# Performance work log

Measured on AMD Instinct MI355X. Metric: run time of the kernel, lower is better.

## Reference

```python
import jax, jax.numpy as jnp
import numpy as np

B, C, N = 8, 256, 4096
K = C // 4  # projection dim for F and G (feat_dim // 4)


def setup_inputs() -> dict:
    key = jax.random.key(0)
    k1, k2, k3, k4, k5, k6 = jax.random.split(key, 6)
    inp = {
        "input": jax.random.normal(k1, (B, C, N), dtype=jnp.float32),
        "nms_feat": jax.random.normal(k2, (B, C, N), dtype=jnp.float32),
        "WF": jax.random.normal(k3, (K, C), dtype=jnp.float32) * (1.0 / np.sqrt(C)),
        "WG": jax.random.normal(k4, (K, C), dtype=jnp.float32) * (1.0 / np.sqrt(C)),
        "WH": jax.random.normal(k5, (C, C), dtype=jnp.float32) * (1.0 / np.sqrt(C)),
        "gamma": jax.random.normal(k6, (1,), dtype=jnp.float32),
    }
    return inp


def reference(input, nms_feat, WF, WG, WH, gamma):
    feat = nms_feat  # [B, C, N]; module uses nms_feat when provided
    b, c, n = feat.shape
    # 1x1 conv projections == channel matmuls; outputs laid out as [B, N, d]
    f = jnp.einsum('kc,bcn->bnk', WF, feat)   # [B, N, K]
    g = jnp.einsum('kc,bcn->bnk', WG, feat)   # [B, N, K]
    h = jnp.einsum('dc,bcn->bnd', WH, feat)   # [B, N, C]
    # attention scores (no scaling in original module)
    s = jnp.einsum('bnk,bmk->bnm', g, f)      # [B, N, N]
    beta = jax.nn.softmax(s, axis=-1)
    o = jnp.einsum('bnm,bmd->bnd', beta, h)   # [B, N, C]
    # NOTE: the original does a raw reshape [B,N,C] -> [B,C,N] (not a transpose);
    # we reproduce that exactly.
    o = o.reshape(b, c, n)
    return gamma * o + input
```

## Files before the change

### kernel.cpp

```cpp
#include <hip/hip_runtime.h>
#include <hip/hip_bf16.h>

#define BB 8
#define CC 256
#define NN 4096
#define KP 64
#define LOG2E 1.44269504088896f

typedef _Float16 f16x8 __attribute__((ext_vector_type(8)));
typedef _Float16 f16x4 __attribute__((ext_vector_type(4)));
typedef float    f32x4 __attribute__((ext_vector_type(4)));

#define MFMA16(a, b, c) __builtin_amdgcn_mfma_f32_16x16x32_f16((a), (b), (c), 0, 0, 0)

__device__ __forceinline__ float fast_exp2(float x) {
#if __has_builtin(__builtin_amdgcn_exp2f)
    return __builtin_amdgcn_exp2f(x);
#else
    return __expf(x * 0.69314718055994531f);
#endif
}

template<int CTRL>
__device__ __forceinline__ float dpp_ror_f(float x) {
    return __int_as_float(__builtin_amdgcn_update_dpp(
        0, __float_as_int(x), CTRL, 0xF, 0xF, true));
}
__device__ __forceinline__ float max16(float x) {
    x = fmaxf(x, dpp_ror_f<0x128>(x));
    x = fmaxf(x, dpp_ror_f<0x124>(x));
    x = fmaxf(x, dpp_ror_f<0x122>(x));
    x = fmaxf(x, dpp_ror_f<0x121>(x));
    return x;
}
__device__ __forceinline__ float sum16(float x) {
    x += dpp_ror_f<0x128>(x);
    x += dpp_ror_f<0x124>(x);
    x += dpp_ror_f<0x122>(x);
    x += dpp_ror_f<0x121>(x);
    return x;
}

__global__ __launch_bounds__(256) void wconv_kernel(
    const float* __restrict__ WF, const float* __restrict__ WG,
    const float* __restrict__ WH, _Float16* __restrict__ W16)
{
    int gid = blockIdx.x * 256 + threadIdx.x;
    int i4  = gid * 4;
    const float* src;
    if (i4 < 64 * CC)        src = WF + i4;
    else if (i4 < 128 * CC)  src = WG + (i4 - 64 * CC);
    else                     src = WH + (i4 - 128 * CC);
    float4 v = *(const float4*)src;
    f16x4 o = { (_Float16)v.x, (_Float16)v.y, (_Float16)v.z, (_Float16)v.w };
    *(f16x4*)(W16 + i4) = o;
}

__global__ __launch_bounds__(256, 3) void proj16_kernel(
    const float* __restrict__ feat, const _Float16* __restrict__ W16,
    _Float16* __restrict__ fb, _Float16* __restrict__ gb,
    _Float16* __restrict__ hT)
{
    __shared__ __align__(16) _Float16 ft[64][264];
    const int b = blockIdx.y, n0 = blockIdx.x * 64, t = threadIdx.x;

    #pragma unroll
    for (int i = 0; i < 16; i++) {
        int v = t + i * 256, c = v >> 4, nq = v & 15;
        float4 x = *(const float4*)(feat + ((size_t)b * CC + c) * NN + n0 + nq * 4);
        ft[nq * 4 + 0][c] = (_Float16)x.x;
        ft[nq * 4 + 1][c] = (_Float16)x.y;
        ft[nq * 4 + 2][c] = (_Float16)x.z;
        ft[nq * 4 + 3][c] = (_Float16)x.w;
    }
    __syncthreads();

    const int w = t >> 6, lane = t & 63, quad = lane >> 4, ln = lane & 15;
    const int rowbase = w * 96;

    f32x4 acc[6][4] = {};
    #pragma unroll
    for (int ks = 0; ks < 8; ks++) {
        const int c0 = ks * 32;
        f16x8 bfr[4];
        #pragma unroll
        for (int tf = 0; tf < 4; tf++)
            bfr[tf] = *(const f16x8*)&ft[tf * 16 + ln][c0 + quad * 8];
        #pragma unroll
        for (int af = 0; af < 6; af++) {
            f16x8 a = *(const f16x8*)(W16 + (size_t)(rowbase + af * 16 + ln) * CC + c0 + quad * 8);
            #pragma unroll
            for (int tf = 0; tf < 4; tf++)
                acc[af][tf] = MFMA16(a, bfr[tf], acc[af][tf]);
        }
    }

    #pragma unroll
    for (int af = 0; af < 6; af++) {
        const int orow0 = rowbase + af * 16 + quad * 4;
        if (orow0 < 64) {
            #pragma unroll
            for (int tf = 0; tf < 4; tf++) {
                const int tok = n0 + tf * 16 + ln;
                f16x4 pk = { (_Float16)acc[af][tf][0], (_Float16)acc[af][tf][1],
                             (_Float16)acc[af][tf][2], (_Float16)acc[af][tf][3] };
                *(f16x4*)(fb + ((size_t)b * NN + tok) * KP + orow0) = pk;
            }
        } else if (orow0 < 128) {
            #pragma unroll
            for (int tf = 0; tf < 4; tf++) {
                const int tok = n0 + tf * 16 + ln;
                f16x4 pk = { (_Float16)(acc[af][tf][0] * LOG2E),
                             (_Float16)(acc[af][tf][1] * LOG2E),
                             (_Float16)(acc[af][tf][2] * LOG2E),
                             (_Float16)(acc[af][tf][3] * LOG2E) };
                *(f16x4*)(gb + ((size_t)b * NN + tok) * KP + (orow0 - 64)) = pk;
            }
        } else {
            #pragma unroll
            for (int r = 0; r < 4; r++) {
                const int d = orow0 - 128 + r;
                f16x4 pk = { (_Float16)acc[af][0][r], (_Float16)acc[af][1][r],
                             (_Float16)acc[af][2][r], (_Float16)acc[af][3][r] };
                *(f16x4*)(hT + ((size_t)b * CC + d) * NN + n0 + ln * 4) = pk;
            }
        }
    }
}

__global__ __launch_bounds__(256, 2) void attn16_kernel(
    const _Float16* __restrict__ fb, const _Float16* __restrict__ gb,
    const _Float16* __restrict__ hT, const float* __restrict__ inp,
    const float* __restrict__ gamma, float* __restrict__ out)
{
    __shared__ __align__(16) _Float16 g_s[64][72];
    __shared__ __align__(16) _Float16 f_s[64][72];
    __shared__ __align__(16) _Float16 p_s[64][72];
    __shared__ float alpha_s[64];
    __shared__ float l_s[64];
    __shared__ float chg_s[4];

    const int b = blockIdx.x, q0 = blockIdx.y * 64, t = threadIdx.x;
    const int w = t >> 6, lane = t & 63, quad = lane >> 4, ln = lane & 15;
    const int row = t >> 2, kq = t & 3;
    const int dbase = w * 64;

    {
        const _Float16* src = gb + ((size_t)b * NN + q0 + row) * KP + kq * 16;
        *(f16x8*)&g_s[row][kq * 16]     = *(const f16x8*)(src);
        *(f16x8*)&g_s[row][kq * 16 + 8] = *(const f16x8*)(src + 8);
    }
    f16x8 fr0, fr1;
    {
        const _Float16* src = fb + ((size_t)b * NN + row) * KP + kq * 16;
        fr0 = *(const f16x8*)(src);
        fr1 = *(const f16x8*)(src + 8);
    }
    __syncthreads();

    f16x8 ag[2];
    ag[0] = *(const f16x8*)&g_s[w * 16 + ln][quad * 8];
    ag[1] = *(const f16x8*)&g_s[w * 16 + ln][32 + quad * 8];

    float m_run[4] = {-1e30f, -1e30f, -1e30f, -1e30f};
    float l_run[4] = {0.f, 0.f, 0.f, 0.f};
    f32x4 acc[4][4] = {};
    f16x8 hv[2][4];

    #pragma unroll 1
    for (int mt = 0; mt < NN / 64; mt++) {
        const int m0 = mt * 64;

        *(f16x8*)&f_s[row][kq * 16]     = fr0;
        *(f16x8*)&f_s[row][kq * 16 + 8] = fr1;
        __syncthreads();

        {
            const int m0n = ((mt + 1) & 63) * 64;
            const _Float16* srcf = fb + ((size_t)b * NN + m0n + row) * KP + kq * 16;
            fr0 = *(const f16x8*)(srcf);
            fr1 = *(const f16x8*)(srcf + 8);
            #pragma unroll
            for (int ks = 0; ks < 2; ks++)
                #pragma unroll
                for (int df = 0; df < 4; df++)
                    hv[ks][df] = *(const f16x8*)(hT +
                        ((size_t)b * CC + dbase + df * 16 + ln) * NN + m0 + ks * 32 + quad * 8);
        }

        f32x4 S[4] = {};
        #pragma unroll
        for (int ks = 0; ks < 2; ks++) {
            #pragma unroll
            for (int mf = 0; mf < 4; mf++) {
                f16x8 bf = *(const f16x8*)&f_s[mf * 16 + ln][ks * 32 + quad * 8];
                S[mf] = MFMA16(ag[ks], bf, S[mf]);
            }
        }

        float pmax[4];
        bool upd = false;
        #pragma unroll
        for (int r = 0; r < 4; r++) {
            pmax[r] = fmaxf(fmaxf(S[0][r], S[1][r]), fmaxf(S[2][r], S[3][r]));
            upd |= (pmax[r] > m_run[r] + 10.0f);
        }
        const bool wave_upd = (__ballot(upd) != 0ull);
        if (wave_upd) {
            #pragma unroll
            for (int r = 0; r < 4; r++) {
                float mx   = max16(pmax[r]);
                float mnew = fmaxf(m_run[r], mx);
                float al   = fast_exp2(m_run[r] - mnew);
                l_run[r] *= al;
                m_run[r]  = mnew;
                if (ln == 0) alpha_s[w * 16 + quad * 4 + r] = al;
            }
        }
        if (lane == 0) chg_s[w] = wave_upd ? 1.0f : 0.0f;
        #pragma unroll
        for (int r = 0; r < 4; r++) {
            float p0 = fast_exp2(S[0][r] - m_run[r]);
            float p1 = fast_exp2(S[1][r] - m_run[r]);
            float p2 = fast_exp2(S[2][r] - m_run[r]);
            float p3 = fast_exp2(S[3][r] - m_run[r]);
            l_run[r] += (p0 + p1) + (p2 + p3);
            f16x4 pk = { (_Float16)p0, (_Float16)p1, (_Float16)p2, (_Float16)p3 };
            *(f16x4*)&p_s[w * 16 + quad * 4 + r][ln * 4] = pk;
        }
        __syncthreads();

        {
            float c0 = chg_s[0], c1 = chg_s[1], c2 = chg_s[2], c3 = chg_s[3];
            float chg[4] = {c0, c1, c2, c3};
            #pragma unroll
            for (int qf = 0; qf < 4; qf++) {
                if (chg[qf] != 0.0f) {
                    #pragma unroll
                    for (int r = 0; r < 4; r++) {
                        float al = alpha_s[qf * 16 + quad * 4 + r];
                        #pragma unroll
                        for (int df = 0; df < 4; df++)
                            acc[qf][df][r] *= al;
                    }
                }
            }
        }

        #pragma unroll
        for (int ks = 0; ks < 2; ks++) {
            #pragma unroll
            for (int qf = 0; qf < 4; qf++) {
                f16x8 ap = *(const f16x8*)&p_s[qf * 16 + ln][ks * 32 + quad * 8];
                #pragma unroll
                for (int df = 0; df < 4; df++)
                    acc[qf][df] = MFMA16(ap, hv[ks][df], acc[qf][df]);
            }
        }
    }

    #pragma unroll
    for (int r = 0; r < 4; r++) {
        float lt = sum16(l_run[r]);
        if (ln == 0) l_s[w * 16 + quad * 4 + r] = lt;
    }
    __syncthreads();

    const float gam = gamma[0];
    #pragma unroll
    for (int qf = 0; qf < 4; qf++) {
        #pragma unroll
        for (int r = 0; r < 4; r++) {
            const int q = qf * 16 + quad * 4 + r;
            const float linv = 1.0f / l_s[q];
            #pragma unroll
            for (int df = 0; df < 4; df++) {
                const int d = dbase + df * 16 + ln;
                size_t idx = ((size_t)b * NN + q0 + q) * CC + d;
                out[idx] = fmaf(gam, acc[qf][df][r] * linv, inp[idx]);
            }
        }
    }
}

extern "C" void kernel_launch(void* const* d_in, const int* in_sizes, int n_in,
                              void* d_out, int out_size, void* d_ws, size_t ws_size,
                              hipStream_t stream) {
    const float* input = (const float*)d_in[0];
    const float* nms   = (const float*)d_in[1];
    const float* WF    = (const float*)d_in[2];
    const float* WG    = (const float*)d_in[3];
    const float* WH    = (const float*)d_in[4];
    const float* gamma = (const float*)d_in[5];
    float* out = (float*)d_out;

    char* ws = (char*)d_ws;
    _Float16* W16  = (_Float16*)ws;
    _Float16* fb16 = (_Float16*)(ws + 196608);
    _Float16* gb16 = (_Float16*)(ws + 196608 + 4194304);
    _Float16* hT16 = (_Float16*)(ws + 196608 + 2 * 4194304);

    wconv_kernel<<<96, 256, 0, stream>>>(WF, WG, WH, W16);
    proj16_kernel<<<dim3(NN / 64, BB), 256, 0, stream>>>(nms, W16, fb16, gb16, hT16);
    attn16_kernel<<<dim3(BB, NN / 64), 256, 0, stream>>>(fb16, gb16, hT16, input, gamma, out);
}
```

Before: 255.9 us.

## Split attention key range across two blocks and merge with log-sum-exp combine

```diff
diff --git a/kernel.cpp b/kernel.cpp
--- a/kernel.cpp
+++ b/kernel.cpp
@@ -128,11 +128,14 @@
     }
 }
 
-__global__ __launch_bounds__(256, 2) void attn16_kernel(
+template<int NSPLIT>
+__global__ __launch_bounds__(256, 4) void attn16_kernel(
     const _Float16* __restrict__ fb, const _Float16* __restrict__ gb,
     const _Float16* __restrict__ hT, const float* __restrict__ inp,
-    const float* __restrict__ gamma, float* __restrict__ out)
+    const float* __restrict__ gamma, float* __restrict__ out,
+    _Float16* __restrict__ oP, float* __restrict__ lseP)
 {
+    constexpr int ITERS = (NN / 64) / NSPLIT;
     __shared__ __align__(16) _Float16 g_s[64][72];
     __shared__ __align__(16) _Float16 f_s[64][72];
     __shared__ __align__(16) _Float16 p_s[64][72];
@@ -141,6 +144,8 @@
     __shared__ float chg_s[4];
 
     const int b = blockIdx.x, q0 = blockIdx.y * 64, t = threadIdx.x;
+    const int z = (NSPLIT > 1) ? blockIdx.z : 0;
+    const int mtbase = z * ITERS;
     const int w = t >> 6, lane = t & 63, quad = lane >> 4, ln = lane & 15;
     const int row = t >> 2, kq = t & 3;
     const int dbase = w * 64;
@@ -152,7 +157,7 @@
     }
     f16x8 fr0, fr1;
     {
-        const _Float16* src = fb + ((size_t)b * NN + row) * KP + kq * 16;
+        const _Float16* src = fb + ((size_t)b * NN + mtbase * 64 + row) * KP + kq * 16;
         fr0 = *(const f16x8*)(src);
         fr1 = *(const f16x8*)(src + 8);
     }
@@ -168,15 +173,15 @@
     f16x8 hv[2][4];
 
     #pragma unroll 1
-    for (int mt = 0; mt < NN / 64; mt++) {
-        const int m0 = mt * 64;
+    for (int mtl = 0; mtl < ITERS; mtl++) {
+        const int m0 = (mtbase + mtl) * 64;
 
         *(f16x8*)&f_s[row][kq * 16]     = fr0;
         *(f16x8*)&f_s[row][kq * 16 + 8] = fr1;
         __syncthreads();
 
         {
-            const int m0n = ((mt + 1) & 63) * 64;
+            const int m0n = (mtbase + ((mtl + 1) & (ITERS - 1))) * 64;
             const _Float16* srcf = fb + ((size_t)b * NN + m0n + row) * KP + kq * 16;
             fr0 = *(const f16x8*)(srcf);
             fr1 = *(const f16x8*)(srcf + 8);
@@ -231,8 +236,7 @@
         __syncthreads();
 
         {
-            float c0 = chg_s[0], c1 = chg_s[1], c2 = chg_s[2], c3 = chg_s[3];
-            float chg[4] = {c0, c1, c2, c3};
+            float chg[4] = { chg_s[0], chg_s[1], chg_s[2], chg_s[3] };
             #pragma unroll
             for (int qf = 0; qf < 4; qf++) {
                 if (chg[qf] != 0.0f) {
@@ -262,25 +266,83 @@
     #pragma unroll
     for (int r = 0; r < 4; r++) {
         float lt = sum16(l_run[r]);
-        if (ln == 0) l_s[w * 16 + quad * 4 + r] = lt;
+        if (ln == 0) {
+            l_s[w * 16 + quad * 4 + r] = lt;
+            if (NSPLIT > 1)
+                lseP[(size_t)z * BB * NN + (size_t)b * NN + q0 + w * 16 + quad * 4 + r]
+                    = m_run[r] + __log2f(lt);
+        }
     }
     __syncthreads();
 
+    if constexpr (NSPLIT == 1) {
+        const float gam = gamma[0];
+        #pragma unroll
+        for (int qf = 0; qf < 4; qf++) {
+            #pragma unroll
+            for (int r = 0; r < 4; r++) {
+                const int q = qf * 16 + quad * 4 + r;
+                const float linv = 1.0f / l_s[q];
+                #pragma unroll
+                for (int df = 0; df < 4; df++) {
+                    const int d = dbase + df * 16 + ln;
+                    size_t idx = ((size_t)b * NN + q0 + q) * CC + d;
+                    out[idx] = fmaf(gam, acc[qf][df][r] * linv, inp[idx]);
+                }
+            }
+        }
+    } else {
+        _Float16* oPz = oP + (size_t)z * BB * NN * CC;
+        #pragma unroll
+        for (int qf = 0; qf < 4; qf++) {
+            #pragma unroll
+            for (int r = 0; r < 4; r++) {
+                const int q = qf * 16 + quad * 4 + r;
+                const float linv = 1.0f / l_s[q];
+                #pragma unroll
+                for (int df = 0; df < 4; df++) {
+                    const int d = dbase + df * 16 + ln;
+                    oPz[((size_t)b * NN + q0 + q) * CC + d] = (_Float16)(acc[qf][df][r] * linv);
+                }
+            }
+        }
+    }
+}
+
+__global__ __launch_bounds__(256) void combine_kernel(
+    const _Float16* __restrict__ oP, const float* __restrict__ lseP,
+    const float* __restrict__ inp, const float* __restrict__ gamma,
+    float* __restrict__ out)
+{
+    const int gid = blockIdx.x * 256 + threadIdx.x;
+    const int rowi = gid >> 5;
+    const int d0 = (gid & 31) * 8;
+    const size_t base = (size_t)rowi * CC + d0;
+
+    float l0 = lseP[rowi];
+    float l1 = lseP[(size_t)BB * NN + rowi];
+    float M  = fmaxf(l0, l1);
+    float w0 = fast_exp2(l0 - M), w1 = fast_exp2(l1 - M);
+    float inv = 1.0f / (w0 + w1);
+    w0 *= inv; w1 *= inv;
+
+    f16x8 a0 = *(const f16x8*)(oP + base);
+    f16x8 a1 = *(const f16x8*)(oP + (size_t)BB * NN * CC + base);
     const float gam = gamma[0];
-    #pragma unroll
-    for (int qf = 0; qf < 4; qf++) {
-        #pragma unroll
-        for (int r = 0; r < 4; r++) {
-            const int q = qf * 16 + quad * 4 + r;
-            const float linv = 1.0f / l_s[q];
-            #pragma unroll
-            for (int df = 0; df < 4; df++) {
-                const int d = dbase + df * 16 + ln;
-                size_t idx = ((size_t)b * NN + q0 + q) * CC + d;
-                out[idx] = fmaf(gam, acc[qf][df][r] * linv, inp[idx]);
-            }
-        }
-    }
+
+    float4 i0 = *(const float4*)(inp + base);
+    float4 i1 = *(const float4*)(inp + base + 4);
+    float4 o0, o1;
+    o0.x = fmaf(gam, w0 * (float)a0[0] + w1 * (float)a1[0], i0.x);
+    o0.y = fmaf(gam, w0 * (float)a0[1] + w1 * (float)a1[1], i0.y);
+    o0.z = fmaf(gam, w0 * (float)a0[2] + w1 * (float)a1[2], i0.z);
+    o0.w = fmaf(gam, w0 * (float)a0[3] + w1 * (float)a1[3], i0.w);
+    o1.x = fmaf(gam, w0 * (float)a0[4] + w1 * (float)a1[4], i1.x);
+    o1.y = fmaf(gam, w0 * (float)a0[5] + w1 * (float)a1[5], i1.y);
+    o1.z = fmaf(gam, w0 * (float)a0[6] + w1 * (float)a1[6], i1.z);
+    o1.w = fmaf(gam, w0 * (float)a0[7] + w1 * (float)a1[7], i1.w);
+    *(float4*)(out + base)     = o0;
+    *(float4*)(out + base + 4) = o1;
 }
 
 extern "C" void kernel_launch(void* const* d_in, const int* in_sizes, int n_in,
@@ -299,8 +361,21 @@
     _Float16* fb16 = (_Float16*)(ws + 196608);
     _Float16* gb16 = (_Float16*)(ws + 196608 + 4194304);
     _Float16* hT16 = (_Float16*)(ws + 196608 + 2 * 4194304);
+    const size_t base_end = 196608 + 2 * 4194304 + (size_t)2 * BB * NN * CC;
+    _Float16* oP   = (_Float16*)(ws + base_end);
+    float*    lseP = (float*)(ws + base_end + (size_t)2 * 2 * BB * NN * CC);
+    const size_t need = base_end + (size_t)2 * 2 * BB * NN * CC + (size_t)2 * 4 * BB * NN;
 
     wconv_kernel<<<96, 256, 0, stream>>>(WF, WG, WH, W16);
     proj16_kernel<<<dim3(NN / 64, BB), 256, 0, stream>>>(nms, W16, fb16, gb16, hT16);
-    attn16_kernel<<<dim3(BB, NN / 64), 256, 0, stream>>>(fb16, gb16, hT16, input, gamma, out);
-}
+
+    if (ws_size >= need) {
+        attn16_kernel<2><<<dim3(BB, NN / 64, 2), 256, 0, stream>>>(
+            fb16, gb16, hT16, input, gamma, out, oP, lseP);
+        combine_kernel<<<(BB * NN * CC / 8) / 256, 256, 0, stream>>>(
+            oP, lseP, input, gamma, out);
+    } else {
+        attn16_kernel<1><<<dim3(BB, NN / 64), 256, 0, stream>>>(
+            fb16, gb16, hT16, input, gamma, out, oP, lseP);
+    }
+}
```

Measured after the change: 552.6 us. 2.16x slower.

## Halve query tile to 32 rows, raise occupancy, split h loads

Applied to the files above, without the earlier changes.

```diff
diff --git a/kernel.cpp b/kernel.cpp
--- a/kernel.cpp
+++ b/kernel.cpp
@@ -128,27 +128,27 @@
     }
 }
 
-__global__ __launch_bounds__(256, 2) void attn16_kernel(
+__global__ __launch_bounds__(256, 4) void attn16_kernel(
     const _Float16* __restrict__ fb, const _Float16* __restrict__ gb,
     const _Float16* __restrict__ hT, const float* __restrict__ inp,
     const float* __restrict__ gamma, float* __restrict__ out)
 {
-    __shared__ __align__(16) _Float16 g_s[64][72];
+    __shared__ __align__(16) _Float16 g_s[32][72];
     __shared__ __align__(16) _Float16 f_s[64][72];
-    __shared__ __align__(16) _Float16 p_s[64][72];
-    __shared__ float alpha_s[64];
-    __shared__ float l_s[64];
-    __shared__ float chg_s[4];
-
-    const int b = blockIdx.x, q0 = blockIdx.y * 64, t = threadIdx.x;
+    __shared__ __align__(16) _Float16 p_s[32][72];
+    __shared__ float alpha_s[32];
+    __shared__ float l_s[32];
+    __shared__ float chg_s[2];
+
+    const int b = blockIdx.x, q0 = blockIdx.y * 32, t = threadIdx.x;
     const int w = t >> 6, lane = t & 63, quad = lane >> 4, ln = lane & 15;
     const int row = t >> 2, kq = t & 3;
     const int dbase = w * 64;
 
     {
-        const _Float16* src = gb + ((size_t)b * NN + q0 + row) * KP + kq * 16;
-        *(f16x8*)&g_s[row][kq * 16]     = *(const f16x8*)(src);
-        *(f16x8*)&g_s[row][kq * 16 + 8] = *(const f16x8*)(src + 8);
+        const int gr = t >> 3, gc = (t & 7) * 8;
+        const _Float16* src = gb + ((size_t)b * NN + q0 + gr) * KP + gc;
+        *(f16x8*)&g_s[gr][gc] = *(const f16x8*)src;
     }
     f16x8 fr0, fr1;
     {
@@ -159,13 +159,15 @@
     __syncthreads();
 
     f16x8 ag[2];
-    ag[0] = *(const f16x8*)&g_s[w * 16 + ln][quad * 8];
-    ag[1] = *(const f16x8*)&g_s[w * 16 + ln][32 + quad * 8];
+    if (w < 2) {
+        ag[0] = *(const f16x8*)&g_s[w * 16 + ln][quad * 8];
+        ag[1] = *(const f16x8*)&g_s[w * 16 + ln][32 + quad * 8];
+    }
 
     float m_run[4] = {-1e30f, -1e30f, -1e30f, -1e30f};
     float l_run[4] = {0.f, 0.f, 0.f, 0.f};
-    f32x4 acc[4][4] = {};
-    f16x8 hv[2][4];
+    f32x4 acc[2][4] = {};
+    f16x8 hv[4];
 
     #pragma unroll 1
     for (int mt = 0; mt < NN / 64; mt++) {
@@ -181,60 +183,59 @@
             fr0 = *(const f16x8*)(srcf);
             fr1 = *(const f16x8*)(srcf + 8);
             #pragma unroll
-            for (int ks = 0; ks < 2; ks++)
+            for (int df = 0; df < 4; df++)
+                hv[df] = *(const f16x8*)(hT +
+                    ((size_t)b * CC + dbase + df * 16 + ln) * NN + m0 + quad * 8);
+        }
+
+        if (w < 2) {
+            f32x4 S[4] = {};
+            #pragma unroll
+            for (int ks = 0; ks < 2; ks++) {
                 #pragma unroll
-                for (int df = 0; df < 4; df++)
-                    hv[ks][df] = *(const f16x8*)(hT +
-                        ((size_t)b * CC + dbase + df * 16 + ln) * NN + m0 + ks * 32 + quad * 8);
-        }
-
-        f32x4 S[4] = {};
-        #pragma unroll
-        for (int ks = 0; ks < 2; ks++) {
-            #pragma unroll
-            for (int mf = 0; mf < 4; mf++) {
-                f16x8 bf = *(const f16x8*)&f_s[mf * 16 + ln][ks * 32 + quad * 8];
-                S[mf] = MFMA16(ag[ks], bf, S[mf]);
-            }
-        }
-
-        float pmax[4];
-        bool upd = false;
-        #pragma unroll
-        for (int r = 0; r < 4; r++) {
-            pmax[r] = fmaxf(fmaxf(S[0][r], S[1][r]), fmaxf(S[2][r], S[3][r]));
-            upd |= (pmax[r] > m_run[r] + 10.0f);
-        }
-        const bool wave_upd = (__ballot(upd) != 0ull);
-        if (wave_upd) {
+                for (int mf = 0; mf < 4; mf++) {
+                    f16x8 bf = *(const f16x8*)&f_s[mf * 16 + ln][ks * 32 + quad * 8];
+                    S[mf] = MFMA16(ag[ks], bf, S[mf]);
+                }
+            }
+
+            float pmax[4];
+            bool upd = false;
             #pragma unroll
             for (int r = 0; r < 4; r++) {
-                float mx   = max16(pmax[r]);
-                float mnew = fmaxf(m_run[r], mx);
-                float al   = fast_exp2(m_run[r] - mnew);
-                l_run[r] *= al;
-                m_run[r]  = mnew;
-                if (ln == 0) alpha_s[w * 16 + quad * 4 + r] = al;
-            }
-        }
-        if (lane == 0) chg_s[w] = wave_upd ? 1.0f : 0.0f;
-        #pragma unroll
-        for (int r = 0; r < 4; r++) {
-            float p0 = fast_exp2(S[0][r] - m_run[r]);
-            float p1 = fast_exp2(S[1][r] - m_run[r]);
-            float p2 = fast_exp2(S[2][r] - m_run[r]);
-            float p3 = fast_exp2(S[3][r] - m_run[r]);
-            l_run[r] += (p0 + p1) + (p2 + p3);
-            f16x4 pk = { (_Float16)p0, (_Float16)p1, (_Float16)p2, (_Float16)p3 };
-            *(f16x4*)&p_s[w * 16 + quad * 4 + r][ln * 4] = pk;
+                pmax[r] = fmaxf(fmaxf(S[0][r], S[1][r]), fmaxf(S[2][r], S[3][r]));
+                upd |= (pmax[r] > m_run[r] + 10.0f);
+            }
+            const bool wave_upd = (__ballot(upd) != 0ull);
+            if (wave_upd) {
+                #pragma unroll
+                for (int r = 0; r < 4; r++) {
+                    float mx   = max16(pmax[r]);
+                    float mnew = fmaxf(m_run[r], mx);
+                    float al   = fast_exp2(m_run[r] - mnew);
+                    l_run[r] *= al;
+                    m_run[r]  = mnew;
+                    if (ln == 0) alpha_s[w * 16 + quad * 4 + r] = al;
+                }
+            }
+            if (lane == 0) chg_s[w] = wave_upd ? 1.0f : 0.0f;
+            #pragma unroll
+            for (int r = 0; r < 4; r++) {
+                float p0 = fast_exp2(S[0][r] - m_run[r]);
+                float p1 = fast_exp2(S[1][r] - m_run[r]);
+                float p2 = fast_exp2(S[2][r] - m_run[r]);
+                float p3 = fast_exp2(S[3][r] - m_run[r]);
+                l_run[r] += (p0 + p1) + (p2 + p3);
+                f16x4 pk = { (_Float16)p0, (_Float16)p1, (_Float16)p2, (_Float16)p3 };
+                *(f16x4*)&p_s[w * 16 + quad * 4 + r][ln * 4] = pk;
+            }
         }
         __syncthreads();
 
         {
-            float c0 = chg_s[0], c1 = chg_s[1], c2 = chg_s[2], c3 = chg_s[3];
-            float chg[4] = {c0, c1, c2, c3};
-            #pragma unroll
-            for (int qf = 0; qf < 4; qf++) {
+            float chg[2] = { chg_s[0], chg_s[1] };
+            #pragma unroll
+            for (int qf = 0; qf < 2; qf++) {
                 if (chg[qf] != 0.0f) {
                     #pragma unroll
                     for (int r = 0; r < 4; r++) {
@@ -248,27 +249,37 @@
         }
 
         #pragma unroll
-        for (int ks = 0; ks < 2; ks++) {
-            #pragma unroll
-            for (int qf = 0; qf < 4; qf++) {
-                f16x8 ap = *(const f16x8*)&p_s[qf * 16 + ln][ks * 32 + quad * 8];
-                #pragma unroll
-                for (int df = 0; df < 4; df++)
-                    acc[qf][df] = MFMA16(ap, hv[ks][df], acc[qf][df]);
-            }
-        }
-    }
-
-    #pragma unroll
-    for (int r = 0; r < 4; r++) {
-        float lt = sum16(l_run[r]);
-        if (ln == 0) l_s[w * 16 + quad * 4 + r] = lt;
+        for (int qf = 0; qf < 2; qf++) {
+            f16x8 ap = *(const f16x8*)&p_s[qf * 16 + ln][quad * 8];
+            #pragma unroll
+            for (int df = 0; df < 4; df++)
+                acc[qf][df] = MFMA16(ap, hv[df], acc[qf][df]);
+        }
+        #pragma unroll
+        for (int df = 0; df < 4; df++)
+            hv[df] = *(const f16x8*)(hT +
+                ((size_t)b * CC + dbase + df * 16 + ln) * NN + m0 + 32 + quad * 8);
+        #pragma unroll
+        for (int qf = 0; qf < 2; qf++) {
+            f16x8 ap = *(const f16x8*)&p_s[qf * 16 + ln][32 + quad * 8];
+            #pragma unroll
+            for (int df = 0; df < 4; df++)
+                acc[qf][df] = MFMA16(ap, hv[df], acc[qf][df]);
+        }
+    }
+
+    if (w < 2) {
+        #pragma unroll
+        for (int r = 0; r < 4; r++) {
+            float lt = sum16(l_run[r]);
+            if (ln == 0) l_s[w * 16 + quad * 4 + r] = lt;
+        }
     }
     __syncthreads();
 
     const float gam = gamma[0];
     #pragma unroll
-    for (int qf = 0; qf < 4; qf++) {
+    for (int qf = 0; qf < 2; qf++) {
         #pragma unroll
         for (int r = 0; r < 4; r++) {
             const int q = qf * 16 + quad * 4 + r;
@@ -302,5 +313,6 @@
 
     wconv_kernel<<<96, 256, 0, stream>>>(WF, WG, WH, W16);
     proj16_kernel<<<dim3(NN / 64, BB), 256, 0, stream>>>(nms, W16, fb16, gb16, hT16);
-    attn16_kernel<<<dim3(BB, NN / 64), 256, 0, stream>>>(fb16, gb16, hT16, input, gamma, out);
-}
+    attn16_kernel<<<dim3(BB, NN / 32), 256, 0, stream>>>(
+        fb16, gb16, hT16, input, gamma, out);
+}
```

After: 372.9 us. 45.7% more time.
